# Kernel optimization log

Measured on AMD Instinct MI355X. Metric: run time of the kernel, lower is better.

Reference implementation:

```python
import jax, jax.numpy as jnp
import numpy as np

CHUNK = 128      # chunk_size
SAMPLE = 16      # sample_size -> at most SAMPLE chunks selected per row


def sinusoidal_pe(T, H):
    # standard transformer sinusoidal positional encoding [T, H]
    pos = jnp.arange(T, dtype=jnp.float32)[:, None]
    div = jnp.exp(jnp.arange(0, H, 2, dtype=jnp.float32) * (-np.log(10000.0) / H))
    pe = jnp.zeros((T, H), dtype=jnp.float32)
    pe = pe.at[:, 0::2].set(jnp.sin(pos * div))
    pe = pe.at[:, 1::2].set(jnp.cos(pos * div))
    return pe


def setup_inputs() -> dict:
    key = jax.random.key(0)
    k1, k2, k3, k4 = jax.random.split(key, 4)
    B, T, D, H = 8, 8192, 1024, 1024
    data = jax.random.normal(k1, (B, T, D), jnp.float32)
    state = jax.random.normal(k2, (B, 64, H), jnp.float32)
    W = jax.random.normal(k3, (D, H), jnp.float32) / np.sqrt(D)
    b = jnp.zeros((H,), jnp.float32)
    chunk_idx = jax.random.randint(k4, (B, SAMPLE), 0, T // CHUNK)  # sampled chunks
    return {"state": state, "data": data, "W": W, "b": b, "chunk_idx": chunk_idx}


def reference(state, data, W, b, chunk_idx):
    B, T, D = data.shape
    H = W.shape[1]
    n_chunks = T // CHUNK
    # add_pos: linear embed + positional encoding, scaled by sqrt(chunk_size)
    x = (data @ W + b + sinusoidal_pe(T, H)[None]) * np.sqrt(CHUNK)  # [B,T,H]
    # union of SAMPLE one-hot chunk selections (== StochasticMultinomialTensor sample .max(1))
    onehot = jax.nn.one_hot(chunk_idx, n_chunks, dtype=jnp.float32)   # [B,SAMPLE,n_chunks]
    mask_c = onehot.max(axis=1)                                       # [B,n_chunks] in {0,1}
    mask = jnp.repeat(mask_c, CHUNK, axis=1)                          # [B,T]
    lens = mask.sum(axis=1).astype(jnp.int32)                         # selected token counts
    # stable left-alignment: selected positions first, original order preserved
    order = jnp.argsort(1.0 - mask, axis=1, stable=True)              # [B,T]
    Smax = SAMPLE * CHUNK                                             # static max length
    order = order[:, :Smax]
    gathered = jnp.take_along_axis(x, order[..., None], axis=1)       # [B,Smax,H]
    valid = (jnp.arange(Smax)[None, :] < lens[:, None]).astype(x.dtype)
    # selected tokens scaled by F value (=1.0); padding zeroed (pad_sequence semantics)
    return gathered * valid[..., None]
```

## Files before the change

### kernel.cpp

```cpp
#include <hip/hip_runtime.h>
#include <hip/hip_fp16.h>
#include <math.h>

#define NB 8
#define NT 8192
#define ND 1024
#define NH 1024
#define CHUNK_ 128
#define SAMPLE_ 16
#define NCHUNK 64
#define SMAX 2048
#define MROWS (NB * SMAX)

typedef _Float16 half8 __attribute__((ext_vector_type(8)));
typedef float floatx4 __attribute__((ext_vector_type(4)));

__device__ __forceinline__ unsigned short f2h(float f) {
  return __half_as_ushort(__float2half(f));
}

__global__ __launch_bounds__(256) void k_select(const int* __restrict__ cidx,
                                                int* __restrict__ srcT) {
  __shared__ int sel[SAMPLE_];
  __shared__ int nsel_s;
  const int b = blockIdx.x;
  if (threadIdx.x == 0) {
    unsigned long long m = 0ull;
    for (int j = 0; j < SAMPLE_; ++j) m |= (1ull << (cidx[b * SAMPLE_ + j] & 63));
    int n = 0;
    for (int c = 0; c < NCHUNK; ++c)
      if ((m >> c) & 1ull) sel[n++] = c;
    nsel_s = n;
  }
  __syncthreads();
  const int n = nsel_s;
  for (int s = threadIdx.x; s < SMAX; s += 256) {
    const int k = s >> 7;
    srcT[b * SMAX + s] = (k < n) ? (sel[k] * CHUNK_ + (s & 127)) : -1;
  }
}

__global__ __launch_bounds__(256) void k_wt(const float* __restrict__ W,
                                            unsigned short* __restrict__ Wt) {
  __shared__ unsigned short tile[64][65];
  const int hb = blockIdx.x * 64;
  const int db = blockIdx.y * 64;
  const int c = threadIdx.x & 63;
  const int r0 = threadIdx.x >> 6;
#pragma unroll
  for (int j = 0; j < 16; ++j) {
    const int r = r0 + j * 4;
    tile[c][r] = f2h(W[(size_t)(db + r) * NH + hb + c]);
  }
  __syncthreads();
#pragma unroll
  for (int j = 0; j < 16; ++j) {
    const int r = r0 + j * 4;
    Wt[(size_t)(hb + r) * ND + db + c] = tile[r][c];
  }
}

__global__ __launch_bounds__(256) void k_gatherA(const float* __restrict__ data,
                                                 const int* __restrict__ srcT,
                                                 unsigned short* __restrict__ A) {
  const int row = blockIdx.x;
  const int t = srcT[row];
  const int d = threadIdx.x * 4;
  ushort4 o;
  if (t < 0) {
    o = make_ushort4(0, 0, 0, 0);
  } else {
    const int b = row >> 11;
    const float4 v = *(const float4*)(data + ((size_t)b * NT + t) * ND + d);
    o.x = f2h(v.x); o.y = f2h(v.y); o.z = f2h(v.z); o.w = f2h(v.w);
  }
  *(ushort4*)(A + (size_t)row * ND + d) = o;
}

__device__ __forceinline__ void gl_lds16(const unsigned short* g, unsigned short* l) {
  __builtin_amdgcn_global_load_lds(
      (const __attribute__((address_space(1))) unsigned int*)g,
      (__attribute__((address_space(3))) unsigned int*)l, 16, 0, 0);
}

__global__ __launch_bounds__(256) void k_gemm(const unsigned short* __restrict__ A,
                                              const unsigned short* __restrict__ Bt,
                                              const float* __restrict__ bias,
                                              const int* __restrict__ srcT,
                                              float* __restrict__ out) {
  __shared__ unsigned short As[128 * 32];
  __shared__ unsigned short Bs[128 * 32];
  __shared__ int tS[128];

  const int tid = threadIdx.x;
  const int tile_n = blockIdx.x & 7;
  const int tile_m = blockIdx.x >> 3;

  if (tid < 128) tS[tid] = srcT[tile_m * 128 + tid];

  const int lane = tid & 63;
  const int wave = tid >> 6;
  const int wm = wave & 1;
  const int wn = wave >> 1;

  floatx4 acc[4][4];
#pragma unroll
  for (int i = 0; i < 4; ++i)
#pragma unroll
    for (int j = 0; j < 4; ++j) acc[i][j] = (floatx4){0.f, 0.f, 0.f, 0.f};

  const int ar = tid >> 2;
  const int ac = (tid & 3) * 8;
  const unsigned short* gA = A + (size_t)(tile_m * 128 + ar) * ND + ac;
  const unsigned short* gB = Bt + (size_t)(tile_n * 128 + ar) * ND + ac;
  unsigned short* lA = As + wave * 512;
  unsigned short* lB = Bs + wave * 512;

  const int aoff = (wm * 64 + (lane & 15)) * 32 + (lane >> 4) * 8;
  const int boff = (wn * 64 + (lane & 15)) * 32 + (lane >> 4) * 8;

  for (int kk = 0; kk < ND; kk += 32) {
    __syncthreads();
    gl_lds16(gA + kk, lA);
    gl_lds16(gA + 64 * ND + kk, lA + 2048);
    gl_lds16(gB + kk, lB);
    gl_lds16(gB + 64 * ND + kk, lB + 2048);
    __syncthreads();

    half8 af[4], bf[4];
#pragma unroll
    for (int i = 0; i < 4; ++i) af[i] = *(const half8*)(As + aoff + i * 16 * 32);
#pragma unroll
    for (int i = 0; i < 4; ++i) bf[i] = *(const half8*)(Bs + boff + i * 16 * 32);
#pragma unroll
    for (int i = 0; i < 4; ++i)
#pragma unroll
      for (int j = 0; j < 4; ++j)
        acc[i][j] = __builtin_amdgcn_mfma_f32_16x16x32_f16(af[i], bf[j], acc[i][j], 0, 0, 0);
  }

  const float scale = 11.313708498984761f;
  const float nl = -9.210340371976184f / 1024.f;
  const int colq = lane & 15;
  const int rq = (lane >> 4) * 4;
#pragma unroll
  for (int j = 0; j < 4; ++j) {
    const int gh = tile_n * 128 + wn * 64 + j * 16 + colq;
    const float freq = __expf((float)(gh & ~1) * nl);
    const float bv = bias[gh];
#pragma unroll
    for (int i = 0; i < 4; ++i) {
      const int lrow0 = wm * 64 + i * 16 + rq;
#pragma unroll
      for (int r = 0; r < 4; ++r) {
        const int lrow = lrow0 + r;
        const int t = tS[lrow];
        float v = 0.0f;
        if (t >= 0) {
          const float arg = (float)t * freq;
          const float pe = (gh & 1) ? __cosf(arg) : __sinf(arg);
          v = (acc[i][j][r] + bv + pe) * scale;
        }
        out[(size_t)(tile_m * 128 + lrow) * NH + gh] = v;
      }
    }
  }
}

extern "C" void kernel_launch(void* const* d_in, const int* in_sizes, int n_in,
                              void* d_out, int out_size, void* d_ws, size_t ws_size,
                              hipStream_t stream) {
  const float* data = (const float*)d_in[1];
  const float* W = (const float*)d_in[2];
  const float* bias = (const float*)d_in[3];
  const int* cidx = (const int*)d_in[4];
  float* out = (float*)d_out;

  char* ws = (char*)d_ws;
  int* srcT = (int*)ws;
  unsigned short* Wt = (unsigned short*)(ws + (64 << 10));
  unsigned short* A = (unsigned short*)(ws + (64 << 10) + (2 << 20));

  k_select<<<NB, 256, 0, stream>>>(cidx, srcT);
  k_wt<<<dim3(NH / 64, ND / 64), 256, 0, stream>>>(W, Wt);
  k_gatherA<<<MROWS, 256, 0, stream>>>(data, srcT, A);
  k_gemm<<<(MROWS / 128) * (NH / 128), 256, 0, stream>>>(A, Wt, bias, srcT, out);
}
```

Baseline: 400.5 us.

## Skip padding chunk tiles in GEMM, widen K tile with swizzled LDS

```diff
diff --git a/kernel.cpp b/kernel.cpp
--- a/kernel.cpp
+++ b/kernel.cpp
@@ -11,9 +11,11 @@
 #define NCHUNK 64
 #define SMAX 2048
 #define MROWS (NB * SMAX)
+#define BK 64
 
 typedef _Float16 half8 __attribute__((ext_vector_type(8)));
 typedef float floatx4 __attribute__((ext_vector_type(4)));
+typedef unsigned short ushort8 __attribute__((ext_vector_type(8)));
 
 __device__ __forceinline__ unsigned short f2h(float f) {
   return __half_as_ushort(__float2half(f));
@@ -63,18 +65,18 @@
 __global__ __launch_bounds__(256) void k_gatherA(const float* __restrict__ data,
                                                  const int* __restrict__ srcT,
                                                  unsigned short* __restrict__ A) {
-  const int row = blockIdx.x;
+  const int row = blockIdx.x * 2 + (threadIdx.x >> 7);
   const int t = srcT[row];
-  const int d = threadIdx.x * 4;
-  ushort4 o;
-  if (t < 0) {
-    o = make_ushort4(0, 0, 0, 0);
-  } else {
-    const int b = row >> 11;
-    const float4 v = *(const float4*)(data + ((size_t)b * NT + t) * ND + d);
-    o.x = f2h(v.x); o.y = f2h(v.y); o.z = f2h(v.z); o.w = f2h(v.w);
-  }
-  *(ushort4*)(A + (size_t)row * ND + d) = o;
+  if (t < 0) return;
+  const int b = row >> 11;
+  const int col = (threadIdx.x & 127) * 8;
+  const float4* src = (const float4*)(data + ((size_t)b * NT + t) * ND + col);
+  const float4 v0 = src[0];
+  const float4 v1 = src[1];
+  ushort8 o;
+  o[0] = f2h(v0.x); o[1] = f2h(v0.y); o[2] = f2h(v0.z); o[3] = f2h(v0.w);
+  o[4] = f2h(v1.x); o[5] = f2h(v1.y); o[6] = f2h(v1.z); o[7] = f2h(v1.w);
+  *(ushort8*)(A + (size_t)row * ND + col) = o;
 }
 
 __device__ __forceinline__ void gl_lds16(const unsigned short* g, unsigned short* l) {
@@ -88,20 +90,28 @@
                                               const float* __restrict__ bias,
                                               const int* __restrict__ srcT,
                                               float* __restrict__ out) {
-  __shared__ unsigned short As[128 * 32];
-  __shared__ unsigned short Bs[128 * 32];
-  __shared__ int tS[128];
+  __shared__ unsigned short As[128 * BK];
+  __shared__ unsigned short Bs[128 * BK];
 
   const int tid = threadIdx.x;
   const int tile_n = blockIdx.x & 7;
   const int tile_m = blockIdx.x >> 3;
-
-  if (tid < 128) tS[tid] = srcT[tile_m * 128 + tid];
+  const int t0 = srcT[tile_m * 128];
+
+  if (t0 < 0) {
+    const int r = tid >> 1;
+    const int cb = (tid & 1) * 64;
+    float4 z = make_float4(0.f, 0.f, 0.f, 0.f);
+    float* o = out + (size_t)(tile_m * 128 + r) * NH + tile_n * 128 + cb;
+#pragma unroll
+    for (int v = 0; v < 16; ++v) *(float4*)(o + 4 * v) = z;
+    return;
+  }
 
   const int lane = tid & 63;
-  const int wave = tid >> 6;
-  const int wm = wave & 1;
-  const int wn = wave >> 1;
+  const int w = tid >> 6;
+  const int wm = w & 1;
+  const int wn = w >> 1;
 
   floatx4 acc[4][4];
 #pragma unroll
@@ -109,34 +119,49 @@
 #pragma unroll
     for (int j = 0; j < 4; ++j) acc[i][j] = (floatx4){0.f, 0.f, 0.f, 0.f};
 
-  const int ar = tid >> 2;
-  const int ac = (tid & 3) * 8;
-  const unsigned short* gA = A + (size_t)(tile_m * 128 + ar) * ND + ac;
-  const unsigned short* gB = Bt + (size_t)(tile_n * 128 + ar) * ND + ac;
-  unsigned short* lA = As + wave * 512;
-  unsigned short* lB = Bs + wave * 512;
-
-  const int aoff = (wm * 64 + (lane & 15)) * 32 + (lane >> 4) * 8;
-  const int boff = (wn * 64 + (lane & 15)) * 32 + (lane >> 4) * 8;
-
-  for (int kk = 0; kk < ND; kk += 32) {
+  const int srow = lane >> 3;
+  const int g8 = (((lane & 7) ^ srow) * 8);
+  const unsigned short* gA0 =
+      A + (size_t)(tile_m * 128 + w * 32 + srow) * ND + g8;
+  const unsigned short* gB0 =
+      Bt + (size_t)(tile_n * 128 + w * 32 + srow) * ND + g8;
+  unsigned short* lA0 = As + w * 2048;
+  unsigned short* lB0 = Bs + w * 2048;
+
+  const int mrow = wm * 64 + (lane & 15);
+  const int nrow = wn * 64 + (lane & 15);
+  const int x7 = lane & 7;
+  int aoff[4][2], boff[4][2];
+#pragma unroll
+  for (int i = 0; i < 4; ++i)
+#pragma unroll
+    for (int s = 0; s < 2; ++s) {
+      const int c = ((lane >> 4) + s * 4) ^ x7;
+      aoff[i][s] = (mrow + i * 16) * BK + c * 8;
+      boff[i][s] = (nrow + i * 16) * BK + c * 8;
+    }
+
+  for (int kk = 0; kk < ND; kk += BK) {
     __syncthreads();
-    gl_lds16(gA + kk, lA);
-    gl_lds16(gA + 64 * ND + kk, lA + 2048);
-    gl_lds16(gB + kk, lB);
-    gl_lds16(gB + 64 * ND + kk, lB + 2048);
+#pragma unroll
+    for (int q = 0; q < 4; ++q) gl_lds16(gA0 + (size_t)q * 8 * ND + kk, lA0 + q * 512);
+#pragma unroll
+    for (int q = 0; q < 4; ++q) gl_lds16(gB0 + (size_t)q * 8 * ND + kk, lB0 + q * 512);
     __syncthreads();
 
-    half8 af[4], bf[4];
-#pragma unroll
-    for (int i = 0; i < 4; ++i) af[i] = *(const half8*)(As + aoff + i * 16 * 32);
-#pragma unroll
-    for (int i = 0; i < 4; ++i) bf[i] = *(const half8*)(Bs + boff + i * 16 * 32);
-#pragma unroll
-    for (int i = 0; i < 4; ++i)
-#pragma unroll
-      for (int j = 0; j < 4; ++j)
-        acc[i][j] = __builtin_amdgcn_mfma_f32_16x16x32_f16(af[i], bf[j], acc[i][j], 0, 0, 0);
+#pragma unroll
+    for (int s = 0; s < 2; ++s) {
+      half8 af[4], bf[4];
+#pragma unroll
+      for (int i = 0; i < 4; ++i) af[i] = *(const half8*)(As + aoff[i][s]);
+#pragma unroll
+      for (int j = 0; j < 4; ++j) bf[j] = *(const half8*)(Bs + boff[j][s]);
+#pragma unroll
+      for (int i = 0; i < 4; ++i)
+#pragma unroll
+        for (int j = 0; j < 4; ++j)
+          acc[i][j] = __builtin_amdgcn_mfma_f32_16x16x32_f16(af[i], bf[j], acc[i][j], 0, 0, 0);
+    }
   }
 
   const float scale = 11.313708498984761f;
@@ -154,14 +179,10 @@
 #pragma unroll
       for (int r = 0; r < 4; ++r) {
         const int lrow = lrow0 + r;
-        const int t = tS[lrow];
-        float v = 0.0f;
-        if (t >= 0) {
-          const float arg = (float)t * freq;
-          const float pe = (gh & 1) ? __cosf(arg) : __sinf(arg);
-          v = (acc[i][j][r] + bv + pe) * scale;
-        }
-        out[(size_t)(tile_m * 128 + lrow) * NH + gh] = v;
+        const float arg = (float)(t0 + lrow) * freq;
+        const float pe = (gh & 1) ? __cosf(arg) : __sinf(arg);
+        out[(size_t)(tile_m * 128 + lrow) * NH + gh] =
+            (acc[i][j][r] + bv + pe) * scale;
       }
     }
   }
@@ -183,6 +204,6 @@
 
   k_select<<<NB, 256, 0, stream>>>(cidx, srcT);
   k_wt<<<dim3(NH / 64, ND / 64), 256, 0, stream>>>(W, Wt);
-  k_gatherA<<<MROWS, 256, 0, stream>>>(data, srcT, A);
+  k_gatherA<<<MROWS / 2, 256, 0, stream>>>(data, srcT, A);
   k_gemm<<<(MROWS / 128) * (NH / 128), 256, 0, stream>>>(A, Wt, bias, srcT, out);
 }
```

Result: faster. 385.1 us (-3.8%).
